# Kernel tuning notes

Hardware: AMD Instinct MI355X
Metric: run time of the kernel (lower is better)

## Reference

```python
import jax, jax.numpy as jnp
import numpy as np

NUM_TREES = 100
TREE_DEPTH = 5
INPUT_DIM = 256
NUM_CLASSES = 64
BATCH = 8192
NUM_NODES = 2 ** TREE_DEPTH - 1   # 31 decision nodes per tree
NUM_LEAVES = 2 ** TREE_DEPTH      # 32 leaves per tree


def setup_inputs() -> dict:
    key = jax.random.key(0)
    k_x, k_w, k_b, k_l = jax.random.split(key, 4)
    x = jax.random.normal(k_x, (BATCH, INPUT_DIM), dtype=jnp.float32)
    # stacked per-tree decision-node params (torch.randn init)
    node_w = jax.random.normal(k_w, (NUM_TREES, NUM_NODES, INPUT_DIM), dtype=jnp.float32)
    node_b = jax.random.normal(k_b, (NUM_TREES, NUM_NODES), dtype=jnp.float32)
    leaves = jax.random.normal(k_l, (NUM_TREES, NUM_LEAVES, NUM_CLASSES), dtype=jnp.float32)
    return {"x": x, "node_w": node_w, "node_b": node_b, "leaves": leaves}


def reference(x, node_w, node_b, leaves):
    # x: [B, D]; node_w: [T, Nn, D]; node_b: [T, Nn]; leaves: [T, Nl, C]
    T = node_w.shape[0]
    B = x.shape[0]
    depth = int(np.log2(leaves.shape[1]))
    idx = jnp.zeros((T, B), dtype=jnp.int32)
    for _ in range(depth):  # small fixed depth loop
        # gather each sample's routing node per tree: [T, B, D] and [T, B]
        w_g = jnp.take_along_axis(node_w, idx[:, :, None], axis=1)
        b_g = jnp.take_along_axis(node_b, idx, axis=1)
        decisions = jax.nn.sigmoid(jnp.einsum('tbd,bd->tb', w_g, x) + b_g)
        idx = 2 * idx + (decisions <= 0.5).astype(jnp.int32)
    # leaf gather: [T, B, C], then forest average over trees -> [B, C]
    tree_preds = jnp.take_along_axis(leaves, idx[:, :, None], axis=1)
    return jnp.mean(tree_preds, axis=0)
```

## Files before the change

kernel.cpp:

```cpp
#include <hip/hip_runtime.h>


typedef __bf16 bf16;
typedef __attribute__((ext_vector_type(8))) __bf16 bf16x8;
typedef __attribute__((ext_vector_type(4))) float f32x4;

#define NTREES 100
#define NB     8192
#define ND     256
#define NNODES 31
#define NLEAF  32
#define NCLS   64
#define TAU    2.0e-3f
#define QCAP   8192

static __device__ __forceinline__ void gload16(const void* g, void* l) {
    __builtin_amdgcn_global_load_lds(
        (const __attribute__((address_space(1))) void*)g,
        (__attribute__((address_space(3))) void*)l, 16, 0, 0);
}

__global__ void prep(const float* __restrict__ x, const float* __restrict__ wf,
                     const float* __restrict__ lv,
                     bf16* __restrict__ xh, bf16* __restrict__ xl,
                     bf16* __restrict__ wimg, bf16* __restrict__ lv16,
                     unsigned int* __restrict__ qcount) {
    if (blockIdx.x == 0 && threadIdx.x == 0) *qcount = 0;
    if (blockIdx.x < 1024) {
        int i = blockIdx.x * 256 + threadIdx.x;
        int m  = i & 15;
        int dq = (i >> 4) & 31;
        int g  = i >> 9;
        const float* src = x + (size_t)(g * 16 + m) * ND + dq * 8;
        bf16x8 h8, l8;
#pragma unroll
        for (int e = 0; e < 8; ++e) {
            float f = src[e];
            bf16 h = (bf16)f;
            h8[e] = h;
            l8[e] = (bf16)(f - (float)h);
        }
        *(bf16x8*)(xh + (size_t)i * 8) = h8;
        *(bf16x8*)(xl + (size_t)i * 8) = l8;
    } else if (blockIdx.x < 1232) {
        int i = (blockIdx.x - 1024) * 256 + threadIdx.x;
        int oct_g = i & 31;
        int row   = (i >> 5) & 127;
        int tg    = i >> 12;
        int tree  = tg * 8 + (row >> 4), node = row & 15;
        bf16x8 h8, l8;
        if (tree < NTREES) {
            const float* src = wf + ((size_t)tree * NNODES + node) * ND + oct_g * 8;
#pragma unroll
            for (int e = 0; e < 8; ++e) {
                float f = src[e];
                bf16 h = (bf16)f;
                h8[e] = h;
                l8[e] = (bf16)(f - (float)h);
            }
        } else {
#pragma unroll
            for (int e = 0; e < 8; ++e) { h8[e] = (bf16)0.f; l8[e] = (bf16)0.f; }
        }
        int kq = oct_g >> 3, oct = oct_g & 7, cp = oct ^ (row & 7);
        size_t b = (size_t)tg * 65536 + (size_t)kq * 16384 + row * 64 + cp * 8;
        *(bf16x8*)(wimg + b)        = h8;
        *(bf16x8*)(wimg + b + 8192) = l8;
    } else {
        int i = (blockIdx.x - 1232) * 256 + threadIdx.x;
        lv16[i] = (bf16)lv[i];
    }
}

__global__ __launch_bounds__(256, 2) void forest_all(
    const bf16* __restrict__ xh, const bf16* __restrict__ xl,
    const bf16* __restrict__ wimg,
    const float* __restrict__ bias,
    unsigned char* __restrict__ idxb,
    unsigned int* __restrict__ qcount, unsigned int* __restrict__ queue)
{
    __shared__ char lds[65536];
    float* scr = (float*)lds;

    const int tid  = threadIdx.x;
    const int wave = tid >> 6;
    const int lane = tid & 63;
    const int m    = lane & 15;
    const int q    = lane >> 4;

    const int lin  = blockIdx.x + gridDim.x * blockIdx.y;
    const int xcd  = lin & 7;
    const int slot = lin >> 3;
    const int mg   = xcd * 4 + (slot / 13);
    const int tg   = slot % 13;

    float biasv[8];
#pragma unroll
    for (int ni = 0; ni < 8; ++ni) {
        int tree = tg * 8 + ni;
        biasv[ni] = (tree < NTREES) ? bias[(size_t)tree * NNODES + m] : 0.f;
    }

    f32x4 acc[4][8];
#pragma unroll
    for (int mi = 0; mi < 4; ++mi)
#pragma unroll
        for (int ni = 0; ni < 8; ++ni)
            acc[mi][ni] = (f32x4){0.f, 0.f, 0.f, 0.f};

    size_t abase[4];
#pragma unroll
    for (int mi = 0; mi < 4; ++mi)
        abase[mi] = (size_t)(mg * 16 + wave * 4 + mi) * 4096 + lane * 8;

    const bf16* wsrc = wimg + (size_t)tg * 65536;

#pragma unroll
    for (int j = 0; j < 8; ++j) {
        int idx = j * 256 + tid;
        gload16(wsrc + idx * 8, lds + idx * 16);
    }
    __syncthreads();

    bf16x8 cah[4], cal[4], nah[4], nal[4];
#pragma unroll
    for (int mi = 0; mi < 4; ++mi) {
        cah[mi] = *(const bf16x8*)(xh + abase[mi]);
        cal[mi] = *(const bf16x8*)(xl + abase[mi]);
    }

#pragma unroll
    for (int kq = 0; kq < 4; ++kq) {
        const char* bufc = lds + (kq & 1) * 32768;
        if (kq < 3) {
            char* bufn = lds + ((kq + 1) & 1) * 32768;
#pragma unroll
            for (int j = 0; j < 8; ++j) {
                int idx = j * 256 + tid;
                gload16(wsrc + (size_t)(kq + 1) * 16384 + idx * 8, bufn + idx * 16);
            }
        }
#pragma unroll
        for (int kkq = 0; kkq < 2; ++kkq) {
            const int kk = kq * 2 + kkq;
            if (kk < 7) {
#pragma unroll
                for (int mi = 0; mi < 4; ++mi) {
                    nah[mi] = *(const bf16x8*)(xh + abase[mi] + (kk + 1) * 512);
                    nal[mi] = *(const bf16x8*)(xl + abase[mi] + (kk + 1) * 512);
                }
            }
#pragma unroll
            for (int ni = 0; ni < 8; ++ni) {
                const int n  = ni * 16 + m;
                const int cp = (kkq * 4 + q) ^ (m & 7);
                bf16x8 bh = *(const bf16x8*)((const bf16*)bufc + n * 64 + cp * 8);
                bf16x8 bl = *(const bf16x8*)((const bf16*)bufc + 8192 + n * 64 + cp * 8);
#pragma unroll
                for (int mi = 0; mi < 4; ++mi) {
                    acc[mi][ni] = __builtin_amdgcn_mfma_f32_16x16x32_bf16(cal[mi], bh, acc[mi][ni], 0, 0, 0);
                    acc[mi][ni] = __builtin_amdgcn_mfma_f32_16x16x32_bf16(cah[mi], bl, acc[mi][ni], 0, 0, 0);
                    acc[mi][ni] = __builtin_amdgcn_mfma_f32_16x16x32_bf16(cah[mi], bh, acc[mi][ni], 0, 0, 0);
                }
            }
#pragma unroll
            for (int mi = 0; mi < 4; ++mi) { cah[mi] = nah[mi]; cal[mi] = nal[mi]; }
        }
        __syncthreads();
    }

    float* ws_ = scr + wave * 1280;
    const int s_l = wave * 64 + lane;
    const int sg  = mg * 256 + s_l;
    unsigned int pk0 = 0, pk1 = 0;
#pragma unroll
    for (int ni = 0; ni < 8; ++ni) {
#pragma unroll
        for (int mi = 0; mi < 4; ++mi)
#pragma unroll
            for (int r = 0; r < 4; ++r)
                ws_[(mi * 16 + q * 4 + r) * 20 + m] = acc[mi][ni][r] + biasv[ni];
        f32x4 z0 = *(f32x4*)&ws_[lane * 20];
        f32x4 z1 = *(f32x4*)&ws_[lane * 20 + 4];
        f32x4 z2 = *(f32x4*)&ws_[lane * 20 + 8];
        f32x4 z3 = *(f32x4*)&ws_[lane * 20 + 12];
        float z[16] = {z0[0], z0[1], z0[2], z0[3], z1[0], z1[1], z1[2], z1[3],
                       z2[0], z2[1], z2[2], z2[3], z3[0], z3[1], z3[2], z3[3]};
        float a0 = z[0];
        bool d0 = a0 <= 0.f;
        float a1 = d0 ? z[1] : z[0];
        bool d1 = a1 <= 0.f;
        float a2 = d0 ? (d1 ? z[3] : z[2]) : (d1 ? z[1] : z[0]);
        bool d2 = a2 <= 0.f;
        float m0 = d2 ? z[1] : z[0], m1 = d2 ? z[3] : z[2];
        float m2 = d2 ? z[5] : z[4], m3 = d2 ? z[7] : z[6];
        float p0 = d1 ? m1 : m0, p1 = d1 ? m3 : m2;
        float a3 = d0 ? p1 : p0;
        bool d3 = a3 <= 0.f;
        float n0 = d3 ? z[1] : z[0],  n1 = d3 ? z[3] : z[2];
        float n2 = d3 ? z[5] : z[4],  n3 = d3 ? z[7] : z[6];
        float n4 = d3 ? z[9] : z[8],  n5 = d3 ? z[11] : z[10];
        float n6 = d3 ? z[13] : z[12], n7 = d3 ? z[15] : z[14];
        float q0 = d2 ? n1 : n0, q1 = d2 ? n3 : n2;
        float q2 = d2 ? n5 : n4, q3 = d2 ? n7 : n6;
        float r0 = d1 ? q1 : q0, r1 = d1 ? q3 : q2;
        float a4 = d0 ? r1 : r0;
        bool d4 = a4 <= 0.f;
        int leaf = ((int)d0 << 4) | ((int)d1 << 3) | ((int)d2 << 2)
                 | ((int)d3 << 1) | (int)d4;
        if (ni < 4) pk0 |= (unsigned)leaf << (8 * ni);
        else        pk1 |= (unsigned)leaf << (8 * (ni - 4));
        float mn = fminf(fminf(fminf(fabsf(a0), fabsf(a1)),
                               fminf(fabsf(a2), fabsf(a3))), fabsf(a4));
        const int tree = tg * 8 + ni;
        if (tree < NTREES && mn < TAU) {
            unsigned int pos = atomicAdd(qcount, 1u);
            if (pos < QCAP)
                queue[pos] = ((unsigned)tree << 13) | (unsigned)sg;
        }
    }
    unsigned char* dst = idxb + (size_t)sg * NTREES + tg * 8;
    *(unsigned int*)dst = pk0;
    if (tg < 12) *(unsigned int*)(dst + 4) = pk1;
}

__global__ void fixup_kernel(const float* __restrict__ x, const float* __restrict__ wf,
                             const float* __restrict__ bias,
                             const unsigned int* __restrict__ qcount,
                             const unsigned int* __restrict__ queue,
                             unsigned char* __restrict__ idxb) {
    const int wid  = (blockIdx.x * 256 + threadIdx.x) >> 6;
    const int lane = threadIdx.x & 63;
    unsigned int n = *qcount;
    if (n > QCAP) n = QCAP;
    for (unsigned int it = wid; it < n; it += 256) {
        unsigned int e = queue[it];
        int t = e >> 13, s = e & 8191;
        const float* xr = x + (size_t)s * ND;
        float4 xv = *(const float4*)(xr + lane * 4);
        int node = 0;
        for (int lvl = 0; lvl < 5; ++lvl) {
            const float* wr = wf + ((size_t)t * NNODES + node) * ND;
            float4 wv = *(const float4*)(wr + lane * 4);
            double zz = (double)xv.x * wv.x + (double)xv.y * wv.y
                      + (double)xv.z * wv.z + (double)xv.w * wv.w;
#pragma unroll
            for (int o = 32; o > 0; o >>= 1) zz += __shfl_xor(zz, o);
            zz += (double)bias[t * NNODES + node];
            node = 2 * node + (zz <= 0.0 ? 1 : 0);
        }
        if (lane == 0) idxb[(size_t)s * NTREES + t] = (unsigned char)node;
    }
}

__global__ void leaf_gather(const unsigned char* __restrict__ idxb,
                            const bf16* __restrict__ lv16,
                            float* __restrict__ out) {
    const int wave = threadIdx.x >> 6;
    const int lane = threadIdx.x & 63;
    const int s = blockIdx.x * 4 + wave;
    unsigned int rw = 0;
    if (lane < 25) rw = *(const unsigned int*)(idxb + (size_t)s * NTREES + lane * 4);
    float acc = 0.f;
#pragma unroll 10
    for (int t = 0; t < NTREES; ++t) {
        unsigned int wrd = __shfl(rw, t >> 2);
        int li = (wrd >> ((t & 3) * 8)) & 255;
        acc += (float)lv16[((size_t)t * NLEAF + li) * NCLS + lane];
    }
    out[(size_t)s * NCLS + lane] = acc * 0.01f;
}

extern "C" void kernel_launch(void* const* d_in, const int* in_sizes, int n_in,
                              void* d_out, int out_size, void* d_ws, size_t ws_size,
                              hipStream_t stream) {
    const float* x  = (const float*)d_in[0];
    const float* nw = (const float*)d_in[1];
    const float* nb = (const float*)d_in[2];
    const float* lv = (const float*)d_in[3];
    float* out = (float*)d_out;

    char* ws = (char*)d_ws;
    bf16* xh   = (bf16*)(ws + 0);
    bf16* xl   = (bf16*)(ws + 4194304);
    bf16* wimg = (bf16*)(ws + 8388608);
    unsigned char* idxb = (unsigned char*)(ws + 10092544);
    bf16* lv16 = (bf16*)(ws + 10911744);
    unsigned int* qcount = (unsigned int*)(ws + 11321344);
    unsigned int* queue  = (unsigned int*)(ws + 11321360);
    if (ws_size < (size_t)11354128) return;

    prep<<<2032, 256, 0, stream>>>(x, nw, lv, xh, xl, wimg, lv16, qcount);
    forest_all<<<dim3(13, 32), 256, 0, stream>>>(
        xh, xl, wimg, nb, idxb, qcount, queue);
    fixup_kernel<<<64, 256, 0, stream>>>(x, nw, nb, qcount, queue, idxb);
    leaf_gather<<<NB / 4, 256, 0, stream>>>(idxb, lv16, out);
}
```

Baseline: 109.3 us.

## Split forest_all work across 512 threads with two M-tiles per wave

Doubles the block to 8 waves, so each wave handles two 16-row M tiles instead of four. This halves accumulator registers and aims for higher occupancy and more latency hiding. The epilogue is reorganised so each lane evaluates four trees for one sample, with the two half-waves splitting the 8 trees, and writes a single packed word. The register double-buffered prefetch of x tiles is dropped in favour of loading them just before use, which risks exposing global-load latency. Each LDS-loaded weight tile is now shared by twice as many waves.

```diff
diff --git a/kernel.cpp b/kernel.cpp
--- a/kernel.cpp
+++ b/kernel.cpp
@@ -72,7 +72,7 @@
     }
 }
 
-__global__ __launch_bounds__(256, 2) void forest_all(
+__global__ __launch_bounds__(512, 4) void forest_all(
     const bf16* __restrict__ xh, const bf16* __restrict__ xl,
     const bf16* __restrict__ wimg,
     const float* __restrict__ bias,
@@ -80,7 +80,6 @@
     unsigned int* __restrict__ qcount, unsigned int* __restrict__ queue)
 {
     __shared__ char lds[65536];
-    float* scr = (float*)lds;
 
     const int tid  = threadIdx.x;
     const int wave = tid >> 6;
@@ -94,40 +93,26 @@
     const int mg   = xcd * 4 + (slot / 13);
     const int tg   = slot % 13;
 
-    float biasv[8];
-#pragma unroll
-    for (int ni = 0; ni < 8; ++ni) {
-        int tree = tg * 8 + ni;
-        biasv[ni] = (tree < NTREES) ? bias[(size_t)tree * NNODES + m] : 0.f;
-    }
-
-    f32x4 acc[4][8];
-#pragma unroll
-    for (int mi = 0; mi < 4; ++mi)
+    f32x4 acc[2][8];
+#pragma unroll
+    for (int mi = 0; mi < 2; ++mi)
 #pragma unroll
         for (int ni = 0; ni < 8; ++ni)
             acc[mi][ni] = (f32x4){0.f, 0.f, 0.f, 0.f};
 
-    size_t abase[4];
-#pragma unroll
-    for (int mi = 0; mi < 4; ++mi)
-        abase[mi] = (size_t)(mg * 16 + wave * 4 + mi) * 4096 + lane * 8;
+    size_t abase[2];
+#pragma unroll
+    for (int mi = 0; mi < 2; ++mi)
+        abase[mi] = (size_t)(mg * 16 + wave * 2 + mi) * 4096 + lane * 8;
 
     const bf16* wsrc = wimg + (size_t)tg * 65536;
 
 #pragma unroll
-    for (int j = 0; j < 8; ++j) {
-        int idx = j * 256 + tid;
+    for (int j = 0; j < 4; ++j) {
+        int idx = j * 512 + tid;
         gload16(wsrc + idx * 8, lds + idx * 16);
     }
     __syncthreads();
-
-    bf16x8 cah[4], cal[4], nah[4], nal[4];
-#pragma unroll
-    for (int mi = 0; mi < 4; ++mi) {
-        cah[mi] = *(const bf16x8*)(xh + abase[mi]);
-        cal[mi] = *(const bf16x8*)(xl + abase[mi]);
-    }
 
 #pragma unroll
     for (int kq = 0; kq < 4; ++kq) {
@@ -135,20 +120,19 @@
         if (kq < 3) {
             char* bufn = lds + ((kq + 1) & 1) * 32768;
 #pragma unroll
-            for (int j = 0; j < 8; ++j) {
-                int idx = j * 256 + tid;
+            for (int j = 0; j < 4; ++j) {
+                int idx = j * 512 + tid;
                 gload16(wsrc + (size_t)(kq + 1) * 16384 + idx * 8, bufn + idx * 16);
             }
         }
 #pragma unroll
         for (int kkq = 0; kkq < 2; ++kkq) {
             const int kk = kq * 2 + kkq;
-            if (kk < 7) {
-#pragma unroll
-                for (int mi = 0; mi < 4; ++mi) {
-                    nah[mi] = *(const bf16x8*)(xh + abase[mi] + (kk + 1) * 512);
-                    nal[mi] = *(const bf16x8*)(xl + abase[mi] + (kk + 1) * 512);
-                }
+            bf16x8 cah[2], cal[2];
+#pragma unroll
+            for (int mi = 0; mi < 2; ++mi) {
+                cah[mi] = *(const bf16x8*)(xh + abase[mi] + kk * 512);
+                cal[mi] = *(const bf16x8*)(xl + abase[mi] + kk * 512);
             }
 #pragma unroll
             for (int ni = 0; ni < 8; ++ni) {
@@ -157,33 +141,42 @@
                 bf16x8 bh = *(const bf16x8*)((const bf16*)bufc + n * 64 + cp * 8);
                 bf16x8 bl = *(const bf16x8*)((const bf16*)bufc + 8192 + n * 64 + cp * 8);
 #pragma unroll
-                for (int mi = 0; mi < 4; ++mi) {
+                for (int mi = 0; mi < 2; ++mi) {
                     acc[mi][ni] = __builtin_amdgcn_mfma_f32_16x16x32_bf16(cal[mi], bh, acc[mi][ni], 0, 0, 0);
                     acc[mi][ni] = __builtin_amdgcn_mfma_f32_16x16x32_bf16(cah[mi], bl, acc[mi][ni], 0, 0, 0);
                     acc[mi][ni] = __builtin_amdgcn_mfma_f32_16x16x32_bf16(cah[mi], bh, acc[mi][ni], 0, 0, 0);
                 }
             }
-#pragma unroll
-            for (int mi = 0; mi < 4; ++mi) { cah[mi] = nah[mi]; cal[mi] = nal[mi]; }
         }
         __syncthreads();
     }
 
-    float* ws_ = scr + wave * 1280;
-    const int s_l = wave * 64 + lane;
-    const int sg  = mg * 256 + s_l;
-    unsigned int pk0 = 0, pk1 = 0;
+    float biasv[8];
 #pragma unroll
     for (int ni = 0; ni < 8; ++ni) {
-#pragma unroll
-        for (int mi = 0; mi < 4; ++mi)
-#pragma unroll
-            for (int r = 0; r < 4; ++r)
-                ws_[(mi * 16 + q * 4 + r) * 20 + m] = acc[mi][ni][r] + biasv[ni];
-        f32x4 z0 = *(f32x4*)&ws_[lane * 20];
-        f32x4 z1 = *(f32x4*)&ws_[lane * 20 + 4];
-        f32x4 z2 = *(f32x4*)&ws_[lane * 20 + 8];
-        f32x4 z3 = *(f32x4*)&ws_[lane * 20 + 12];
+        int tree = tg * 8 + ni;
+        biasv[ni] = (tree < NTREES) ? bias[(size_t)tree * NNODES + m] : 0.f;
+    }
+
+    float* ws_ = (float*)lds + wave * 1408;
+    const int p = lane >> 5;
+    const int r = lane & 31;
+    const int sg = mg * 256 + wave * 32 + r;
+    unsigned int pk = 0;
+#pragma unroll
+    for (int j = 0; j < 4; ++j) {
+#pragma unroll
+        for (int mi = 0; mi < 2; ++mi)
+#pragma unroll
+            for (int rr = 0; rr < 4; ++rr) {
+                int row = mi * 16 + q * 4 + rr;
+                ws_[row * 44 + m]      = acc[mi][j][rr]     + biasv[j];
+                ws_[row * 44 + 20 + m] = acc[mi][j + 4][rr] + biasv[j + 4];
+            }
+        f32x4 z0 = *(f32x4*)&ws_[r * 44 + p * 20];
+        f32x4 z1 = *(f32x4*)&ws_[r * 44 + p * 20 + 4];
+        f32x4 z2 = *(f32x4*)&ws_[r * 44 + p * 20 + 8];
+        f32x4 z3 = *(f32x4*)&ws_[r * 44 + p * 20 + 12];
         float z[16] = {z0[0], z0[1], z0[2], z0[3], z1[0], z1[1], z1[2], z1[3],
                        z2[0], z2[1], z2[2], z2[3], z3[0], z3[1], z3[2], z3[3]};
         float a0 = z[0];
@@ -208,20 +201,18 @@
         bool d4 = a4 <= 0.f;
         int leaf = ((int)d0 << 4) | ((int)d1 << 3) | ((int)d2 << 2)
                  | ((int)d3 << 1) | (int)d4;
-        if (ni < 4) pk0 |= (unsigned)leaf << (8 * ni);
-        else        pk1 |= (unsigned)leaf << (8 * (ni - 4));
+        pk |= (unsigned)leaf << (8 * j);
         float mn = fminf(fminf(fminf(fabsf(a0), fabsf(a1)),
                                fminf(fabsf(a2), fabsf(a3))), fabsf(a4));
-        const int tree = tg * 8 + ni;
+        const int tree = tg * 8 + (j + p * 4);
         if (tree < NTREES && mn < TAU) {
             unsigned int pos = atomicAdd(qcount, 1u);
             if (pos < QCAP)
                 queue[pos] = ((unsigned)tree << 13) | (unsigned)sg;
         }
     }
-    unsigned char* dst = idxb + (size_t)sg * NTREES + tg * 8;
-    *(unsigned int*)dst = pk0;
-    if (tg < 12) *(unsigned int*)(dst + 4) = pk1;
+    if (tg < 12 || p == 0)
+        *(unsigned int*)(idxb + (size_t)sg * NTREES + tg * 8 + p * 4) = pk;
 }
 
 __global__ void fixup_kernel(const float* __restrict__ x, const float* __restrict__ wf,
@@ -291,7 +282,7 @@
     if (ws_size < (size_t)11354128) return;
 
     prep<<<2032, 256, 0, stream>>>(x, nw, lv, xh, xl, wimg, lv16, qcount);
-    forest_all<<<dim3(13, 32), 256, 0, stream>>>(
+    forest_all<<<dim3(13, 32), 512, 0, stream>>>(
         xh, xl, wimg, nb, idxb, qcount, queue);
     fixup_kernel<<<64, 256, 0, stream>>>(x, nw, nb, qcount, queue, idxb);
     leaf_gather<<<NB / 4, 256, 0, stream>>>(idxb, lv16, out);
```

Result: no change. 108.4 us (median of 2 runs) (-0.9%).

## Fuse bf16 split conversion and near-threshold fixup into forest kernel

Applied to the files above, without the earlier changes.

Removes the separate prep kernel by converting x and node weights from fp32 to hi/lo bf16 pairs inside the GEMM kernel. Weights are now staged to LDS with register loads instead of async global-to-LDS copies. The queued fixup kernel is replaced by an inline fp64 recompute of near-zero node logits, and the leaf gather reads fp32 leaves directly. This cuts two launches, the intermediate workspace traffic and the atomics, but adds conversion ALU work and less overlapped weight staging in the main kernel, plus divergent fp64 work in the epilogue.

```diff
diff --git a/kernel.cpp b/kernel.cpp
--- a/kernel.cpp
+++ b/kernel.cpp
@@ -12,75 +12,41 @@
 #define NLEAF  32
 #define NCLS   64
 #define TAU    2.0e-3f
-#define QCAP   8192
-
-static __device__ __forceinline__ void gload16(const void* g, void* l) {
-    __builtin_amdgcn_global_load_lds(
-        (const __attribute__((address_space(1))) void*)g,
-        (__attribute__((address_space(3))) void*)l, 16, 0, 0);
-}
-
-__global__ void prep(const float* __restrict__ x, const float* __restrict__ wf,
-                     const float* __restrict__ lv,
-                     bf16* __restrict__ xh, bf16* __restrict__ xl,
-                     bf16* __restrict__ wimg, bf16* __restrict__ lv16,
-                     unsigned int* __restrict__ qcount) {
-    if (blockIdx.x == 0 && threadIdx.x == 0) *qcount = 0;
-    if (blockIdx.x < 1024) {
-        int i = blockIdx.x * 256 + threadIdx.x;
-        int m  = i & 15;
-        int dq = (i >> 4) & 31;
-        int g  = i >> 9;
-        const float* src = x + (size_t)(g * 16 + m) * ND + dq * 8;
-        bf16x8 h8, l8;
-#pragma unroll
-        for (int e = 0; e < 8; ++e) {
-            float f = src[e];
-            bf16 h = (bf16)f;
-            h8[e] = h;
-            l8[e] = (bf16)(f - (float)h);
-        }
-        *(bf16x8*)(xh + (size_t)i * 8) = h8;
-        *(bf16x8*)(xl + (size_t)i * 8) = l8;
-    } else if (blockIdx.x < 1232) {
-        int i = (blockIdx.x - 1024) * 256 + threadIdx.x;
-        int oct_g = i & 31;
-        int row   = (i >> 5) & 127;
-        int tg    = i >> 12;
-        int tree  = tg * 8 + (row >> 4), node = row & 15;
-        bf16x8 h8, l8;
-        if (tree < NTREES) {
-            const float* src = wf + ((size_t)tree * NNODES + node) * ND + oct_g * 8;
-#pragma unroll
-            for (int e = 0; e < 8; ++e) {
-                float f = src[e];
-                bf16 h = (bf16)f;
-                h8[e] = h;
-                l8[e] = (bf16)(f - (float)h);
-            }
-        } else {
-#pragma unroll
-            for (int e = 0; e < 8; ++e) { h8[e] = (bf16)0.f; l8[e] = (bf16)0.f; }
-        }
-        int kq = oct_g >> 3, oct = oct_g & 7, cp = oct ^ (row & 7);
-        size_t b = (size_t)tg * 65536 + (size_t)kq * 16384 + row * 64 + cp * 8;
-        *(bf16x8*)(wimg + b)        = h8;
-        *(bf16x8*)(wimg + b + 8192) = l8;
-    } else {
-        int i = (blockIdx.x - 1232) * 256 + threadIdx.x;
-        lv16[i] = (bf16)lv[i];
-    }
+
+static __device__ __forceinline__ int traverse(const float z[16], float* mn_out) {
+    float a0 = z[0];
+    bool d0 = a0 <= 0.f;
+    float a1 = d0 ? z[1] : z[0];
+    bool d1 = a1 <= 0.f;
+    float a2 = d0 ? (d1 ? z[3] : z[2]) : (d1 ? z[1] : z[0]);
+    bool d2 = a2 <= 0.f;
+    float m0 = d2 ? z[1] : z[0], m1 = d2 ? z[3] : z[2];
+    float m2 = d2 ? z[5] : z[4], m3 = d2 ? z[7] : z[6];
+    float p0 = d1 ? m1 : m0, p1 = d1 ? m3 : m2;
+    float a3 = d0 ? p1 : p0;
+    bool d3 = a3 <= 0.f;
+    float n0 = d3 ? z[1] : z[0],  n1 = d3 ? z[3] : z[2];
+    float n2 = d3 ? z[5] : z[4],  n3 = d3 ? z[7] : z[6];
+    float n4 = d3 ? z[9] : z[8],  n5 = d3 ? z[11] : z[10];
+    float n6 = d3 ? z[13] : z[12], n7 = d3 ? z[15] : z[14];
+    float q0 = d2 ? n1 : n0, q1 = d2 ? n3 : n2;
+    float q2 = d2 ? n5 : n4, q3 = d2 ? n7 : n6;
+    float r0 = d1 ? q1 : q0, r1 = d1 ? q3 : q2;
+    float a4 = d0 ? r1 : r0;
+    bool d4 = a4 <= 0.f;
+    *mn_out = fminf(fminf(fminf(fabsf(a0), fabsf(a1)),
+                          fminf(fabsf(a2), fabsf(a3))), fabsf(a4));
+    return ((int)d0 << 4) | ((int)d1 << 3) | ((int)d2 << 2)
+         | ((int)d3 << 1) | (int)d4;
 }
 
 __global__ __launch_bounds__(256, 2) void forest_all(
-    const bf16* __restrict__ xh, const bf16* __restrict__ xl,
-    const bf16* __restrict__ wimg,
+    const float* __restrict__ x,
+    const float* __restrict__ wf,
     const float* __restrict__ bias,
-    unsigned char* __restrict__ idxb,
-    unsigned int* __restrict__ qcount, unsigned int* __restrict__ queue)
+    unsigned char* __restrict__ idxb)
 {
     __shared__ char lds[65536];
-    float* scr = (float*)lds;
 
     const int tid  = threadIdx.x;
     const int wave = tid >> 6;
@@ -94,13 +60,6 @@
     const int mg   = xcd * 4 + (slot / 13);
     const int tg   = slot % 13;
 
-    float biasv[8];
-#pragma unroll
-    for (int ni = 0; ni < 8; ++ni) {
-        int tree = tg * 8 + ni;
-        biasv[ni] = (tree < NTREES) ? bias[(size_t)tree * NNODES + m] : 0.f;
-    }
-
     f32x4 acc[4][8];
 #pragma unroll
     for (int mi = 0; mi < 4; ++mi)
@@ -108,54 +67,77 @@
         for (int ni = 0; ni < 8; ++ni)
             acc[mi][ni] = (f32x4){0.f, 0.f, 0.f, 0.f};
 
-    size_t abase[4];
-#pragma unroll
-    for (int mi = 0; mi < 4; ++mi)
-        abase[mi] = (size_t)(mg * 16 + wave * 4 + mi) * 4096 + lane * 8;
-
-    const bf16* wsrc = wimg + (size_t)tg * 65536;
-
-#pragma unroll
-    for (int j = 0; j < 8; ++j) {
-        int idx = j * 256 + tid;
-        gload16(wsrc + idx * 8, lds + idx * 16);
+    const float* xbase = x + (size_t)(mg * 256 + wave * 64 + m) * ND + q * 8;
+
+    auto stage = [&](int kq, char* buf) {
+#pragma unroll
+        for (int it = 0; it < 4; ++it) {
+            int idx = it * 256 + tid;
+            int oct = idx & 7, row = idx >> 3;
+            int tree = tg * 8 + (row >> 4), node = row & 15;
+            f32x4 v0 = (f32x4){0.f, 0.f, 0.f, 0.f};
+            f32x4 v1 = (f32x4){0.f, 0.f, 0.f, 0.f};
+            if (tree < NTREES) {
+                const float* src = wf + ((size_t)tree * NNODES + node) * ND
+                                 + kq * 64 + oct * 8;
+                v0 = *(const f32x4*)src;
+                v1 = *(const f32x4*)(src + 4);
+            }
+            bf16x8 h8, l8;
+#pragma unroll
+            for (int e = 0; e < 4; ++e) {
+                bf16 h0 = (bf16)v0[e];
+                h8[e]     = h0; l8[e]     = (bf16)(v0[e] - (float)h0);
+                bf16 h1 = (bf16)v1[e];
+                h8[4 + e] = h1; l8[4 + e] = (bf16)(v1[e] - (float)h1);
+            }
+            int cp = oct ^ (row & 7);
+            bf16* dst = (bf16*)buf + row * 64 + cp * 8;
+            *(bf16x8*)dst = h8;
+            *(bf16x8*)(dst + 8192) = l8;
+        }
+    };
+
+    stage(0, lds);
+    f32x4 raw[4][2];
+#pragma unroll
+    for (int mi = 0; mi < 4; ++mi) {
+        raw[mi][0] = *(const f32x4*)(xbase + mi * 4096);
+        raw[mi][1] = *(const f32x4*)(xbase + mi * 4096 + 4);
     }
     __syncthreads();
 
-    bf16x8 cah[4], cal[4], nah[4], nal[4];
-#pragma unroll
-    for (int mi = 0; mi < 4; ++mi) {
-        cah[mi] = *(const bf16x8*)(xh + abase[mi]);
-        cal[mi] = *(const bf16x8*)(xl + abase[mi]);
-    }
-
+    bf16x8 cah[4], cal[4];
 #pragma unroll
     for (int kq = 0; kq < 4; ++kq) {
-        const char* bufc = lds + (kq & 1) * 32768;
-        if (kq < 3) {
-            char* bufn = lds + ((kq + 1) & 1) * 32768;
-#pragma unroll
-            for (int j = 0; j < 8; ++j) {
-                int idx = j * 256 + tid;
-                gload16(wsrc + (size_t)(kq + 1) * 16384 + idx * 8, bufn + idx * 16);
-            }
-        }
+        const bf16* bufc = (const bf16*)(lds + (kq & 1) * 32768);
+        if (kq < 3) stage(kq + 1, lds + ((kq + 1) & 1) * 32768);
 #pragma unroll
         for (int kkq = 0; kkq < 2; ++kkq) {
             const int kk = kq * 2 + kkq;
+#pragma unroll
+            for (int mi = 0; mi < 4; ++mi) {
+#pragma unroll
+                for (int e = 0; e < 4; ++e) {
+                    float f0 = raw[mi][0][e], f1 = raw[mi][1][e];
+                    bf16 h0 = (bf16)f0, h1 = (bf16)f1;
+                    cah[mi][e]     = h0; cal[mi][e]     = (bf16)(f0 - (float)h0);
+                    cah[mi][4 + e] = h1; cal[mi][4 + e] = (bf16)(f1 - (float)h1);
+                }
+            }
             if (kk < 7) {
 #pragma unroll
                 for (int mi = 0; mi < 4; ++mi) {
-                    nah[mi] = *(const bf16x8*)(xh + abase[mi] + (kk + 1) * 512);
-                    nal[mi] = *(const bf16x8*)(xl + abase[mi] + (kk + 1) * 512);
+                    raw[mi][0] = *(const f32x4*)(xbase + mi * 4096 + (kk + 1) * 32);
+                    raw[mi][1] = *(const f32x4*)(xbase + mi * 4096 + (kk + 1) * 32 + 4);
                 }
             }
 #pragma unroll
             for (int ni = 0; ni < 8; ++ni) {
                 const int n  = ni * 16 + m;
                 const int cp = (kkq * 4 + q) ^ (m & 7);
-                bf16x8 bh = *(const bf16x8*)((const bf16*)bufc + n * 64 + cp * 8);
-                bf16x8 bl = *(const bf16x8*)((const bf16*)bufc + 8192 + n * 64 + cp * 8);
+                bf16x8 bh = *(const bf16x8*)(bufc + n * 64 + cp * 8);
+                bf16x8 bl = *(const bf16x8*)(bufc + 8192 + n * 64 + cp * 8);
 #pragma unroll
                 for (int mi = 0; mi < 4; ++mi) {
                     acc[mi][ni] = __builtin_amdgcn_mfma_f32_16x16x32_bf16(cal[mi], bh, acc[mi][ni], 0, 0, 0);
@@ -163,15 +145,19 @@
                     acc[mi][ni] = __builtin_amdgcn_mfma_f32_16x16x32_bf16(cah[mi], bh, acc[mi][ni], 0, 0, 0);
                 }
             }
-#pragma unroll
-            for (int mi = 0; mi < 4; ++mi) { cah[mi] = nah[mi]; cal[mi] = nal[mi]; }
         }
         __syncthreads();
     }
 
-    float* ws_ = scr + wave * 1280;
-    const int s_l = wave * 64 + lane;
-    const int sg  = mg * 256 + s_l;
+    float biasv[8];
+#pragma unroll
+    for (int ni = 0; ni < 8; ++ni) {
+        int tree = tg * 8 + ni;
+        biasv[ni] = (tree < NTREES) ? bias[(size_t)tree * NNODES + m] : 0.f;
+    }
+
+    float* ws_ = (float*)lds + wave * 1280;
+    const int sg = mg * 256 + wave * 64 + lane;
     unsigned int pk0 = 0, pk1 = 0;
 #pragma unroll
     for (int ni = 0; ni < 8; ++ni) {
@@ -186,75 +172,47 @@
         f32x4 z3 = *(f32x4*)&ws_[lane * 20 + 12];
         float z[16] = {z0[0], z0[1], z0[2], z0[3], z1[0], z1[1], z1[2], z1[3],
                        z2[0], z2[1], z2[2], z2[3], z3[0], z3[1], z3[2], z3[3]};
-        float a0 = z[0];
-        bool d0 = a0 <= 0.f;
-        float a1 = d0 ? z[1] : z[0];
-        bool d1 = a1 <= 0.f;
-        float a2 = d0 ? (d1 ? z[3] : z[2]) : (d1 ? z[1] : z[0]);
-        bool d2 = a2 <= 0.f;
-        float m0 = d2 ? z[1] : z[0], m1 = d2 ? z[3] : z[2];
-        float m2 = d2 ? z[5] : z[4], m3 = d2 ? z[7] : z[6];
-        float p0 = d1 ? m1 : m0, p1 = d1 ? m3 : m2;
-        float a3 = d0 ? p1 : p0;
-        bool d3 = a3 <= 0.f;
-        float n0 = d3 ? z[1] : z[0],  n1 = d3 ? z[3] : z[2];
-        float n2 = d3 ? z[5] : z[4],  n3 = d3 ? z[7] : z[6];
-        float n4 = d3 ? z[9] : z[8],  n5 = d3 ? z[11] : z[10];
-        float n6 = d3 ? z[13] : z[12], n7 = d3 ? z[15] : z[14];
-        float q0 = d2 ? n1 : n0, q1 = d2 ? n3 : n2;
-        float q2 = d2 ? n5 : n4, q3 = d2 ? n7 : n6;
-        float r0 = d1 ? q1 : q0, r1 = d1 ? q3 : q2;
-        float a4 = d0 ? r1 : r0;
-        bool d4 = a4 <= 0.f;
-        int leaf = ((int)d0 << 4) | ((int)d1 << 3) | ((int)d2 << 2)
-                 | ((int)d3 << 1) | (int)d4;
+        float mn;
+        int leaf = traverse(z, &mn);
+        const int tree = tg * 8 + ni;
+        if (tree < NTREES && mn < TAU) {
+            const float* xr = x + (size_t)sg * ND;
+            float zc[16];
+#pragma unroll
+            for (int nd = 0; nd < 16; ++nd) zc[nd] = z[nd];
+#pragma unroll
+            for (int nd = 0; nd < 16; ++nd) {
+                if (fabsf(z[nd]) < TAU) {
+                    const float* wr = wf + ((size_t)tree * NNODES + nd) * ND;
+                    double s0 = 0.0, s1 = 0.0;
+#pragma unroll 4
+                    for (int k2 = 0; k2 < 32; ++k2) {
+                        f32x4 xv = *(const f32x4*)(xr + k2 * 8);
+                        f32x4 wv = *(const f32x4*)(wr + k2 * 8);
+                        f32x4 xu = *(const f32x4*)(xr + k2 * 8 + 4);
+                        f32x4 wu = *(const f32x4*)(wr + k2 * 8 + 4);
+                        s0 += (double)xv[0] * wv[0] + (double)xv[1] * wv[1]
+                            + (double)xv[2] * wv[2] + (double)xv[3] * wv[3];
+                        s1 += (double)xu[0] * wu[0] + (double)xu[1] * wu[1]
+                            + (double)xu[2] * wu[2] + (double)xu[3] * wu[3];
+                    }
+                    double zt = s0 + s1 + (double)bias[(size_t)tree * NNODES + nd];
+                    zc[nd] = (zt <= 0.0) ? -1.f : 1.f;
+                }
+            }
+            float mn2;
+            leaf = traverse(zc, &mn2);
+        }
         if (ni < 4) pk0 |= (unsigned)leaf << (8 * ni);
         else        pk1 |= (unsigned)leaf << (8 * (ni - 4));
-        float mn = fminf(fminf(fminf(fabsf(a0), fabsf(a1)),
-                               fminf(fabsf(a2), fabsf(a3))), fabsf(a4));
-        const int tree = tg * 8 + ni;
-        if (tree < NTREES && mn < TAU) {
-            unsigned int pos = atomicAdd(qcount, 1u);
-            if (pos < QCAP)
-                queue[pos] = ((unsigned)tree << 13) | (unsigned)sg;
-        }
     }
     unsigned char* dst = idxb + (size_t)sg * NTREES + tg * 8;
     *(unsigned int*)dst = pk0;
     if (tg < 12) *(unsigned int*)(dst + 4) = pk1;
 }
 
-__global__ void fixup_kernel(const float* __restrict__ x, const float* __restrict__ wf,
-                             const float* __restrict__ bias,
-                             const unsigned int* __restrict__ qcount,
-                             const unsigned int* __restrict__ queue,
-                             unsigned char* __restrict__ idxb) {
-    const int wid  = (blockIdx.x * 256 + threadIdx.x) >> 6;
-    const int lane = threadIdx.x & 63;
-    unsigned int n = *qcount;
-    if (n > QCAP) n = QCAP;
-    for (unsigned int it = wid; it < n; it += 256) {
-        unsigned int e = queue[it];
-        int t = e >> 13, s = e & 8191;
-        const float* xr = x + (size_t)s * ND;
-        float4 xv = *(const float4*)(xr + lane * 4);
-        int node = 0;
-        for (int lvl = 0; lvl < 5; ++lvl) {
-            const float* wr = wf + ((size_t)t * NNODES + node) * ND;
-            float4 wv = *(const float4*)(wr + lane * 4);
-            double zz = (double)xv.x * wv.x + (double)xv.y * wv.y
-                      + (double)xv.z * wv.z + (double)xv.w * wv.w;
-#pragma unroll
-            for (int o = 32; o > 0; o >>= 1) zz += __shfl_xor(zz, o);
-            zz += (double)bias[t * NNODES + node];
-            node = 2 * node + (zz <= 0.0 ? 1 : 0);
-        }
-        if (lane == 0) idxb[(size_t)s * NTREES + t] = (unsigned char)node;
-    }
-}
-
 __global__ void leaf_gather(const unsigned char* __restrict__ idxb,
-                            const bf16* __restrict__ lv16,
+                            const float* __restrict__ lv,
                             float* __restrict__ out) {
     const int wave = threadIdx.x >> 6;
     const int lane = threadIdx.x & 63;
@@ -266,7 +224,7 @@
     for (int t = 0; t < NTREES; ++t) {
         unsigned int wrd = __shfl(rw, t >> 2);
         int li = (wrd >> ((t & 3) * 8)) & 255;
-        acc += (float)lv16[((size_t)t * NLEAF + li) * NCLS + lane];
+        acc += lv[((size_t)t * NLEAF + li) * NCLS + lane];
     }
     out[(size_t)s * NCLS + lane] = acc * 0.01f;
 }
@@ -280,19 +238,9 @@
     const float* lv = (const float*)d_in[3];
     float* out = (float*)d_out;
 
-    char* ws = (char*)d_ws;
-    bf16* xh   = (bf16*)(ws + 0);
-    bf16* xl   = (bf16*)(ws + 4194304);
-    bf16* wimg = (bf16*)(ws + 8388608);
-    unsigned char* idxb = (unsigned char*)(ws + 10092544);
-    bf16* lv16 = (bf16*)(ws + 10911744);
-    unsigned int* qcount = (unsigned int*)(ws + 11321344);
-    unsigned int* queue  = (unsigned int*)(ws + 11321360);
-    if (ws_size < (size_t)11354128) return;
-
-    prep<<<2032, 256, 0, stream>>>(x, nw, lv, xh, xl, wimg, lv16, qcount);
-    forest_all<<<dim3(13, 32), 256, 0, stream>>>(
-        xh, xl, wimg, nb, idxb, qcount, queue);
-    fixup_kernel<<<64, 256, 0, stream>>>(x, nw, nb, qcount, queue, idxb);
-    leaf_gather<<<NB / 4, 256, 0, stream>>>(idxb, lv16, out);
-}
+    unsigned char* idxb = (unsigned char*)d_ws;
+    if (ws_size < (size_t)NB * NTREES) return;
+
+    forest_all<<<dim3(13, 32), 256, 0, stream>>>(x, nw, nb, idxb);
+    leaf_gather<<<NB / 4, 256, 0, stream>>>(idxb, lv, out);
+}
```

Measured after the change: 111.1 us. About the same (+1.6%).
